# Kernel optimization log

Hardware: AMD Instinct MI355X
Metric: run time of the kernel (lower is better)

The kernel has to match this reference:

```python
import jax, jax.numpy as jnp
import numpy as np

EMBED_DIM = 768
NUM_HEADS = 12
HEAD_DIM = EMBED_DIM // NUM_HEADS


def setup_inputs() -> dict:
    key = jax.random.key(0)
    ks = jax.random.split(key, 9)
    s = 1.0 / np.sqrt(EMBED_DIM)
    inp = {
        "x": jax.random.normal(ks[0], (4, 2048, EMBED_DIM), dtype=jnp.float32),
        "W_q": jax.random.uniform(ks[1], (EMBED_DIM, EMBED_DIM), jnp.float32, -s, s),
        "b_q": jax.random.uniform(ks[2], (EMBED_DIM,), jnp.float32, -s, s),
        "W_k": jax.random.uniform(ks[3], (EMBED_DIM, EMBED_DIM), jnp.float32, -s, s),
        "b_k": jax.random.uniform(ks[4], (EMBED_DIM,), jnp.float32, -s, s),
        "W_v": jax.random.uniform(ks[5], (EMBED_DIM, EMBED_DIM), jnp.float32, -s, s),
        "b_v": jax.random.uniform(ks[6], (EMBED_DIM,), jnp.float32, -s, s),
        "W_out": jax.random.uniform(ks[7], (EMBED_DIM, EMBED_DIM), jnp.float32, -s, s),
        "b_out": jax.random.uniform(ks[8], (EMBED_DIM,), jnp.float32, -s, s),
    }
    return inp


def reference(x, W_q, b_q, W_k, b_k, W_v, b_v, W_out, b_out):
    B, N, D = x.shape
    H, Hd = NUM_HEADS, HEAD_DIM
    scale = 1.0 / jnp.sqrt(jnp.asarray(Hd, x.dtype))
    # QKV projections (torch Linear: x @ W.T + b)
    Q = (x @ W_q.T + b_q).reshape(B, N, H, Hd).transpose(0, 2, 1, 3)  # (B,H,N,Hd)
    K = (x @ W_k.T + b_k).reshape(B, N, H, Hd).transpose(0, 2, 1, 3)
    V = (x @ W_v.T + b_v).reshape(B, N, H, Hd).transpose(0, 2, 1, 3)
    scores = jnp.einsum("bhqd,bhkd->bhqk", Q, K) * scale  # (B,H,N,N)
    attn = jax.nn.softmax(scores, axis=-1)
    out = jnp.einsum("bhqk,bhkd->bhqd", attn, V)  # (B,H,N,Hd)
    out = out.transpose(0, 2, 1, 3).reshape(B, N, D)
    return out @ W_out.T + b_out
```

## Files before the change

### kernel.cpp

```cpp
#include <hip/hip_runtime.h>
#include <math.h>

#define D_EMB 768
#define SEQN 2048
#define NB 4
#define NH 12
#define HDIM 64
#define MTOT (NB*SEQN)
#define SCLQ 0.18033688011112042f

typedef unsigned int u32;
typedef unsigned short u16;
typedef short sh4 __attribute__((ext_vector_type(4)));
typedef short bf16x8 __attribute__((ext_vector_type(8)));
typedef float f32x16 __attribute__((ext_vector_type(16)));

#define MFMA32(a,b,c) __builtin_amdgcn_mfma_f32_32x32x16_bf16((a),(b),(c),0,0,0)

__device__ __forceinline__ u32 cvtpk(float a, float b){
    u32 r; asm("v_cvt_pk_bf16_f32 %0, %1, %2" : "=v"(r) : "v"(a), "v"(b)); return r;
}
__device__ __forceinline__ u32 pack_split(float v){
    u32 h = cvtpk(v, v);
    float hf = __builtin_bit_cast(float, h << 16);
    float r = v - hf;
    u32 l = cvtpk(r, r);
    return __builtin_amdgcn_perm(l, h, 0x05040100u);
}
__device__ __forceinline__ void unpack4(uint4 p, sh4& hi, sh4& lo){
    u32 h0 = __builtin_amdgcn_perm(p.y, p.x, 0x05040100u);
    u32 h1 = __builtin_amdgcn_perm(p.w, p.z, 0x05040100u);
    u32 l0 = __builtin_amdgcn_perm(p.y, p.x, 0x07060302u);
    u32 l1 = __builtin_amdgcn_perm(p.w, p.z, 0x07060302u);
    uint2 h = {h0, h1}, l = {l0, l1};
    hi = __builtin_bit_cast(sh4, h);
    lo = __builtin_bit_cast(sh4, l);
}
__device__ __forceinline__ bf16x8 ldfrag(const short* p){
    sh4 a = *(const sh4*)p;
    sh4 b = *(const sh4*)(p+4);
    return __builtin_shufflevector(a,b,0,1,2,3,4,5,6,7);
}

__global__ __launch_bounds__(256) void pack_bf(const float* __restrict__ s, u16* __restrict__ d, int n4){
    int i = blockIdx.x*256 + threadIdx.x;
    if (i >= n4) return;
    float4 v = ((const float4*)s)[i];
    uint2 o = { cvtpk(v.x, v.y), cvtpk(v.z, v.w) };
    ((uint2*)d)[i] = o;
}
__global__ __launch_bounds__(256) void pack_wbf(const float* __restrict__ w0, const float* __restrict__ w1,
                                                const float* __restrict__ w2, const float* __restrict__ w3,
                                                u16* __restrict__ d, int n4){
    const int z = blockIdx.y;
    const float* s = (z==0)?w0:(z==1)?w1:(z==2)?w2:w3;
    int i = blockIdx.x*256 + threadIdx.x;
    if (i >= n4) return;
    float4 v = ((const float4*)s)[i];
    uint2 o = { cvtpk(v.x, v.y), cvtpk(v.z, v.w) };
    ((uint2*)(d + (size_t)z*n4*4))[i] = o;
}

#define GPAD 36

__global__ __launch_bounds__(256,3) void gemm_qkv(const u16* __restrict__ X, const u16* __restrict__ Wb,
        const float* __restrict__ bq, const float* __restrict__ bk, const float* __restrict__ bv,
        u16* __restrict__ oq, u16* __restrict__ okk, u16* __restrict__ ov){
    __shared__ __align__(16) short Ahi[128][GPAD];
    __shared__ __align__(16) short Bhi[128][GPAD];

    const int tid = threadIdx.x;
    const int l = tid & 63, w = tid >> 6;
    const int lq = l & 31, g = l >> 5;
    const int wm = w >> 1, wn = w & 1;
    const int m0 = blockIdx.x * 128;
    const int n0 = blockIdx.y * 128;
    const int z  = blockIdx.z;
    const u16* W = Wb + (size_t)z * D_EMB * D_EMB;
    const float* bias = (z==0) ? bq : (z==1) ? bk : bv;
    u16* out = (z==0) ? oq : (z==1) ? okk : ov;

    f32x16 acc[2][2];
    #pragma unroll
    for (int i=0;i<2;i++)
        #pragma unroll
        for (int j=0;j<2;j++)
            #pragma unroll
            for (int r=0;r<16;r++) acc[i][j][r] = 0.f;

    const int srow = tid >> 1;
    const int skb  = (tid & 1) * 16;
    const u16* ap0 = X + (size_t)(m0+srow)*D_EMB + skb;
    const u16* wp0 = W + (size_t)(n0+srow)*D_EMB + skb;

    uint4 a0 = *(const uint4*)ap0, a1 = *(const uint4*)(ap0+8);
    uint4 w0 = *(const uint4*)wp0, w1 = *(const uint4*)(wp0+8);

    for (int k0 = 0; k0 < D_EMB; k0 += 32) {
        __syncthreads();
        {
            uint2 t;
            t.x=a0.x; t.y=a0.y; *(uint2*)&Ahi[srow][skb]    = t;
            t.x=a0.z; t.y=a0.w; *(uint2*)&Ahi[srow][skb+4]  = t;
            t.x=a1.x; t.y=a1.y; *(uint2*)&Ahi[srow][skb+8]  = t;
            t.x=a1.z; t.y=a1.w; *(uint2*)&Ahi[srow][skb+12] = t;
            t.x=w0.x; t.y=w0.y; *(uint2*)&Bhi[srow][skb]    = t;
            t.x=w0.z; t.y=w0.w; *(uint2*)&Bhi[srow][skb+4]  = t;
            t.x=w1.x; t.y=w1.y; *(uint2*)&Bhi[srow][skb+8]  = t;
            t.x=w1.z; t.y=w1.w; *(uint2*)&Bhi[srow][skb+12] = t;
        }
        if (k0 + 32 < D_EMB){
            const u16* ap = ap0 + k0 + 32;
            const u16* wp = wp0 + k0 + 32;
            a0 = *(const uint4*)ap; a1 = *(const uint4*)(ap+8);
            w0 = *(const uint4*)wp; w1 = *(const uint4*)(wp+8);
        }
        __syncthreads();
        #pragma unroll
        for (int kk=0;kk<2;kk++){
            const int kc = kk*16 + g*8;
            bf16x8 ah[2], bh[2];
            #pragma unroll
            for (int i=0;i<2;i++) ah[i] = ldfrag(&Ahi[wm*64+32*i+lq][kc]);
            #pragma unroll
            for (int j=0;j<2;j++) bh[j] = ldfrag(&Bhi[wn*64+32*j+lq][kc]);
            #pragma unroll
            for (int i=0;i<2;i++)
                #pragma unroll
                for (int j=0;j<2;j++)
                    acc[i][j] = MFMA32(ah[i], bh[j], acc[i][j]);
        }
    }

    #pragma unroll
    for (int j=0;j<2;j++){
        const int c = n0 + wn*64 + 32*j + lq;
        const float bv2 = bias[c];
        #pragma unroll
        for (int i=0;i<2;i++){
            #pragma unroll
            for (int r=0;r<16;r++){
                const int m = m0 + wm*64 + 32*i + (r&3) + 8*(r>>2) + 4*g;
                float v = acc[i][j][r] + bv2;
                if (z==0) v *= SCLQ;
                const int b = m >> 11, n = m & 2047, h = c >> 6, hd = c & 63;
                out[(((size_t)(b*NH + h))*SEQN + n)*HDIM + hd] = (u16)cvtpk(v, v);
            }
        }
    }
}

__global__ __launch_bounds__(256,3) void gemm_out(const u32* __restrict__ A, const u16* __restrict__ Wb,
        const float* __restrict__ bo, float* __restrict__ outp){
    __shared__ __align__(16) short Ahi[128][GPAD];
    __shared__ __align__(16) short Alo[128][GPAD];
    __shared__ __align__(16) short Bhi[128][GPAD];

    const int tid = threadIdx.x;
    const int l = tid & 63, w = tid >> 6;
    const int lq = l & 31, g = l >> 5;
    const int wm = w >> 1, wn = w & 1;
    const int m0 = blockIdx.x * 128;
    const int n0 = blockIdx.y * 128;
    const u16* W = Wb + (size_t)3 * D_EMB * D_EMB;

    f32x16 acc[2][2];
    #pragma unroll
    for (int i=0;i<2;i++)
        #pragma unroll
        for (int j=0;j<2;j++)
            #pragma unroll
            for (int r=0;r<16;r++) acc[i][j][r] = 0.f;

    const int srow = tid >> 1;
    const int skb  = (tid & 1) * 16;
    const u32* ap0 = A + (size_t)(m0+srow)*D_EMB + skb;
    const u16* wp0 = W + (size_t)(n0+srow)*D_EMB + skb;

    uint4 areg[4];
    uint4 w0 = *(const uint4*)wp0, w1 = *(const uint4*)(wp0+8);
    #pragma unroll
    for (int c=0;c<4;c++) areg[c] = *(const uint4*)(ap0 + 4*c);

    for (int k0 = 0; k0 < D_EMB; k0 += 32) {
        __syncthreads();
        #pragma unroll
        for (int c=0;c<4;c++){
            sh4 h, lo2; unpack4(areg[c], h, lo2);
            *(sh4*)&Ahi[srow][skb+4*c] = h;
            *(sh4*)&Alo[srow][skb+4*c] = lo2;
        }
        {
            uint2 t;
            t.x=w0.x; t.y=w0.y; *(uint2*)&Bhi[srow][skb]    = t;
            t.x=w0.z; t.y=w0.w; *(uint2*)&Bhi[srow][skb+4]  = t;
            t.x=w1.x; t.y=w1.y; *(uint2*)&Bhi[srow][skb+8]  = t;
            t.x=w1.z; t.y=w1.w; *(uint2*)&Bhi[srow][skb+12] = t;
        }
        if (k0 + 32 < D_EMB){
            const u32* ap = ap0 + k0 + 32;
            const u16* wp = wp0 + k0 + 32;
            #pragma unroll
            for (int c=0;c<4;c++) areg[c] = *(const uint4*)(ap + 4*c);
            w0 = *(const uint4*)wp; w1 = *(const uint4*)(wp+8);
        }
        __syncthreads();
        #pragma unroll
        for (int kk=0;kk<2;kk++){
            const int kc = kk*16 + g*8;
            bf16x8 ah[2], al[2], bh[2];
            #pragma unroll
            for (int i=0;i<2;i++){
                ah[i] = ldfrag(&Ahi[wm*64+32*i+lq][kc]);
                al[i] = ldfrag(&Alo[wm*64+32*i+lq][kc]);
            }
            #pragma unroll
            for (int j=0;j<2;j++) bh[j] = ldfrag(&Bhi[wn*64+32*j+lq][kc]);
            #pragma unroll
            for (int i=0;i<2;i++)
                #pragma unroll
                for (int j=0;j<2;j++){
                    acc[i][j] = MFMA32(ah[i], bh[j], acc[i][j]);
                    acc[i][j] = MFMA32(al[i], bh[j], acc[i][j]);
                }
        }
    }

    #pragma unroll
    for (int j=0;j<2;j++){
        const int c = n0 + wn*64 + 32*j + lq;
        const float bv2 = bo[c];
        #pragma unroll
        for (int i=0;i<2;i++){
            #pragma unroll
            for (int r=0;r<16;r++){
                const int m = m0 + wm*64 + 32*i + (r&3) + 8*(r>>2) + 4*g;
                outp[(size_t)m*D_EMB + c] = acc[i][j][r] + bv2;
            }
        }
    }
}

#define KB 64
#define KPAD 68
#define NT (SEQN/KB)

__global__ __launch_bounds__(256,2) void attn_bf(const u16* __restrict__ Qg,
                                                 const u16* __restrict__ Kg,
                                                 const u16* __restrict__ Vg,
                                                 u32* __restrict__ Og) {
    __shared__ __align__(16) short Khi[2][KB][KPAD];
    __shared__ __align__(16) short Vthi[2][HDIM][KPAD];

    const int tid = threadIdx.x;
    const int l = tid & 63, w = tid >> 6;
    const int lq = l & 31, g = l >> 5;
    const int qt = blockIdx.x;
    const int bh = blockIdx.y;
    const size_t base = (size_t)bh * SEQN * HDIM;
    const int qrowA = qt*256 + w*64 + lq;
    const int qrowB = qrowA + 32;

    const int key = tid >> 2, dblk = (tid & 3) * 16;
    const int hd = tid & 63, kg = tid >> 6;
    const u16* kp0 = Kg + base + (size_t)key*HDIM + dblk;
    const u16* vp0 = Vg + base + (size_t)(kg*16)*HDIM + hd;

    bf16x8 qhA[4], qhB[4];
    {
        const u16* qpA = Qg + base + (size_t)qrowA*HDIM;
        const u16* qpB = Qg + base + (size_t)qrowB*HDIM;
        #pragma unroll
        for (int kk=0;kk<4;kk++){
            qhA[kk] = __builtin_bit_cast(bf16x8, *(const uint4*)(qpA + kk*16 + g*8));
            qhB[kk] = __builtin_bit_cast(bf16x8, *(const uint4*)(qpB + kk*16 + g*8));
        }
    }

    f32x16 oA0, oA1, oB0, oB1, zro;
    #pragma unroll
    for (int r=0;r<16;r++){ oA0[r]=0.f; oA1[r]=0.f; oB0[r]=0.f; oB1[r]=0.f; zro[r]=0.f; }
    float2 lrA = {0.f, 0.f}, lrB = {0.f, 0.f};

    uint4 kra, krb;
    u32 vt[16];

    auto loadTile = [&](int t){
        const u16* kp = kp0 + (size_t)t*KB*HDIM;
        const u16* vp = vp0 + (size_t)t*KB*HDIM;
        kra = *(const uint4*)kp;
        krb = *(const uint4*)(kp+8);
        #pragma unroll
        for (int i2=0;i2<16;i2++) vt[i2] = vp[(size_t)i2*HDIM];
    };
    auto stageWrite = [&](int cb){
        uint2 t;
        t.x=kra.x; t.y=kra.y; *(uint2*)&Khi[cb][key][dblk]    = t;
        t.x=kra.z; t.y=kra.w; *(uint2*)&Khi[cb][key][dblk+4]  = t;
        t.x=krb.x; t.y=krb.y; *(uint2*)&Khi[cb][key][dblk+8]  = t;
        t.x=krb.z; t.y=krb.w; *(uint2*)&Khi[cb][key][dblk+12] = t;
        #pragma unroll
        for (int c=0;c<4;c++){
            uint2 v2;
            v2.x = __builtin_amdgcn_perm(vt[4*c+1], vt[4*c+0], 0x05040100u);
            v2.y = __builtin_amdgcn_perm(vt[4*c+3], vt[4*c+2], 0x05040100u);
            *(uint2*)&Vthi[cb][hd][kg*16+4*c] = v2;
        }
    };

    loadTile(0);
    stageWrite(0);
    loadTile(1);

    for (int kt=0; kt<NT; kt++){
        const int cb = kt & 1;
        __syncthreads();
        if (kt+1 < NT){
            stageWrite(cb^1);
            if (kt+2 < NT) loadTile(kt+2);
        }

        #pragma unroll
        for (int kb=0; kb<2; kb++){
            f32x16 sA, sB;
            __builtin_amdgcn_s_setprio(1);
            {
                bf16x8 a = ldfrag(&Khi[cb][kb*32+lq][g*8]);
                sA = MFMA32(a, qhA[0], zro);
                sB = MFMA32(a, qhB[0], zro);
            }
            #pragma unroll
            for (int kk=1;kk<4;kk++){
                bf16x8 a = ldfrag(&Khi[cb][kb*32+lq][kk*16 + g*8]);
                sA = MFMA32(a, qhA[kk], sA);
                sB = MFMA32(a, qhB[kk], sB);
            }
            __builtin_amdgcn_s_setprio(0);

            #pragma unroll
            for (int r=0;r<16;r++){ sA[r] = __builtin_amdgcn_exp2f(sA[r]); sB[r] = __builtin_amdgcn_exp2f(sB[r]); }
            #pragma unroll
            for (int r=0;r<16;r+=2){
                float2 a2 = {sA[r], sA[r+1]};
                float2 b2 = {sB[r], sB[r+1]};
                lrA += a2;
                lrB += b2;
            }

            u32 pkA[8], pkB[8];
            #pragma unroll
            for (int j=0;j<8;j++){
                pkA[j] = cvtpk(sA[2*j], sA[2*j+1]);
                pkB[j] = cvtpk(sB[2*j], sB[2*j+1]);
            }
            u32 nA0[4], nA1[4], nB0[4], nB1[4];
            #pragma unroll
            for (int a2=0;a2<2;a2++){
                #pragma unroll
                for (int c=0;c<2;c++){
                    u32 x0 = pkA[4*a2+c], y0 = pkA[4*a2+2+c];
                    asm("v_permlane32_swap_b32 %0, %1" : "+v"(x0), "+v"(y0));
                    nA0[2*a2+c] = x0; nA1[2*a2+c] = y0;
                    u32 x1 = pkB[4*a2+c], y1 = pkB[4*a2+2+c];
                    asm("v_permlane32_swap_b32 %0, %1" : "+v"(x1), "+v"(y1));
                    nB0[2*a2+c] = x1; nB1[2*a2+c] = y1;
                }
            }

            __builtin_amdgcn_s_setprio(1);
            #pragma unroll
            for (int t2=0; t2<2; t2++){
                const int kk = 2*kb + t2;
                uint4 wAv = { nA0[2*t2], nA0[2*t2+1], nA1[2*t2], nA1[2*t2+1] };
                uint4 wBv = { nB0[2*t2], nB0[2*t2+1], nB1[2*t2], nB1[2*t2+1] };
                bf16x8 pbA = __builtin_bit_cast(bf16x8, wAv);
                bf16x8 pbB = __builtin_bit_cast(bf16x8, wBv);
                const int kc = kk*16 + g*8;
                bf16x8 v0h = ldfrag(&Vthi[cb][lq][kc]);
                bf16x8 v1h = ldfrag(&Vthi[cb][32+lq][kc]);
                oA0 = MFMA32(v0h, pbA, oA0);
                oA1 = MFMA32(v1h, pbA, oA1);
                oB0 = MFMA32(v0h, pbB, oB0);
                oB1 = MFMA32(v1h, pbB, oB1);
            }
            __builtin_amdgcn_s_setprio(0);
        }
    }

    const int b = bh / NH, h = bh % NH;
    {
        float lA = lrA.x + lrA.y;
        lA += __shfl_xor(lA, 32);
        const float inv = 1.f / lA;
        u32* op = Og + ((size_t)(b*SEQN + qrowA))*D_EMB + h*HDIM;
        #pragma unroll
        for (int rq=0; rq<4; rq++){
            uint4 w0, w1;
            w0.x = pack_split(oA0[4*rq+0]*inv); w0.y = pack_split(oA0[4*rq+1]*inv);
            w0.z = pack_split(oA0[4*rq+2]*inv); w0.w = pack_split(oA0[4*rq+3]*inv);
            w1.x = pack_split(oA1[4*rq+0]*inv); w1.y = pack_split(oA1[4*rq+1]*inv);
            w1.z = pack_split(oA1[4*rq+2]*inv); w1.w = pack_split(oA1[4*rq+3]*inv);
            *(uint4*)(op + 8*rq + 4*g)      = w0;
            *(uint4*)(op + 32 + 8*rq + 4*g) = w1;
        }
    }
    {
        float lB = lrB.x + lrB.y;
        lB += __shfl_xor(lB, 32);
        const float inv = 1.f / lB;
        u32* op = Og + ((size_t)(b*SEQN + qrowB))*D_EMB + h*HDIM;
        #pragma unroll
        for (int rq=0; rq<4; rq++){
            uint4 w0, w1;
            w0.x = pack_split(oB0[4*rq+0]*inv); w0.y = pack_split(oB0[4*rq+1]*inv);
            w0.z = pack_split(oB0[4*rq+2]*inv); w0.w = pack_split(oB0[4*rq+3]*inv);
            w1.x = pack_split(oB1[4*rq+0]*inv); w1.y = pack_split(oB1[4*rq+1]*inv);
            w1.z = pack_split(oB1[4*rq+2]*inv); w1.w = pack_split(oB1[4*rq+3]*inv);
            *(uint4*)(op + 8*rq + 4*g)      = w0;
            *(uint4*)(op + 32 + 8*rq + 4*g) = w1;
        }
    }
}

extern "C" void kernel_launch(void* const* d_in, const int* in_sizes, int n_in,
                              void* d_out, int out_size, void* d_ws, size_t ws_size,
                              hipStream_t stream) {
    const float* x  = (const float*)d_in[0];
    const float* Wq = (const float*)d_in[1];
    const float* bq = (const float*)d_in[2];
    const float* Wk = (const float*)d_in[3];
    const float* bk = (const float*)d_in[4];
    const float* Wv = (const float*)d_in[5];
    const float* bv = (const float*)d_in[6];
    const float* Wo = (const float*)d_in[7];
    const float* bo = (const float*)d_in[8];

    const size_t per = (size_t)NB*NH*SEQN*HDIM;
    const size_t wplane = (size_t)D_EMB*D_EMB;
    u16* base16 = (u16*)d_ws;
    u16* Xbf = base16;
    u16* Qb  = base16 + per;
    u16* Kb  = base16 + 2*per;
    u16* Vb  = base16 + 3*per;
    u16* Wbf = base16 + 4*per;
    u32* ATpk = (u32*)(base16 + 4*per + 4*wplane);

    pack_bf<<<dim3((int)(per/4/256)), dim3(256), 0, stream>>>(x, Xbf, (int)(per/4));
    pack_wbf<<<dim3(576,4), dim3(256), 0, stream>>>(Wq, Wk, Wv, Wo, Wbf, (int)(wplane/4));

    gemm_qkv<<<dim3(MTOT/128, D_EMB/128, 3), dim3(256), 0, stream>>>(Xbf, Wbf, bq, bk, bv, Qb, Kb, Vb);

    attn_bf<<<dim3(SEQN/256, NB*NH), dim3(256), 0, stream>>>(Qb, Kb, Vb, ATpk);

    gemm_out<<<dim3(MTOT/128, D_EMB/128), dim3(256), 0, stream>>>(ATpk, Wbf, bo, (float*)d_out);
}
```

Measured before the change: 165.1 us.

## Split key tile across wave pairs in attention and reduce partial outputs via LDS

Each block now covers 128 query rows instead of 256. Pairs of waves share the same query rows, and each wave of a pair handles one 32-key half of every 64-key tile. At the end, partial O accumulators and row sums are reduced through shared memory before normalising and writing. This doubles the grid to 768 blocks and raises launch bounds to 3 blocks per SM, aiming for better occupancy and CU fill. In exchange, K/V tile loads are amortised over fewer queries, and an extra LDS reduction with syncs is added.

```diff
diff --git a/kernel.cpp b/kernel.cpp
--- a/kernel.cpp
+++ b/kernel.cpp
@@ -245,7 +245,7 @@
 #define KPAD 68
 #define NT (SEQN/KB)
 
-__global__ __launch_bounds__(256,2) void attn_bf(const u16* __restrict__ Qg,
+__global__ __launch_bounds__(256,3) void attn_bf(const u16* __restrict__ Qg,
                                                  const u16* __restrict__ Kg,
                                                  const u16* __restrict__ Vg,
                                                  u32* __restrict__ Og) {
@@ -255,10 +255,12 @@
     const int tid = threadIdx.x;
     const int l = tid & 63, w = tid >> 6;
     const int lq = l & 31, g = l >> 5;
+    const int khalf = w & 1;
+    const int pair  = w >> 1;
     const int qt = blockIdx.x;
     const int bh = blockIdx.y;
     const size_t base = (size_t)bh * SEQN * HDIM;
-    const int qrowA = qt*256 + w*64 + lq;
+    const int qrowA = qt*128 + pair*64 + lq;
     const int qrowB = qrowA + 32;
 
     const int key = tid >> 2, dblk = (tid & 3) * 16;
@@ -320,104 +322,130 @@
             if (kt+2 < NT) loadTile(kt+2);
         }
 
-        #pragma unroll
-        for (int kb=0; kb<2; kb++){
-            f32x16 sA, sB;
-            __builtin_amdgcn_s_setprio(1);
-            {
-                bf16x8 a = ldfrag(&Khi[cb][kb*32+lq][g*8]);
-                sA = MFMA32(a, qhA[0], zro);
-                sB = MFMA32(a, qhB[0], zro);
-            }
-            #pragma unroll
-            for (int kk=1;kk<4;kk++){
-                bf16x8 a = ldfrag(&Khi[cb][kb*32+lq][kk*16 + g*8]);
-                sA = MFMA32(a, qhA[kk], sA);
-                sB = MFMA32(a, qhB[kk], sB);
-            }
-            __builtin_amdgcn_s_setprio(0);
-
-            #pragma unroll
-            for (int r=0;r<16;r++){ sA[r] = __builtin_amdgcn_exp2f(sA[r]); sB[r] = __builtin_amdgcn_exp2f(sB[r]); }
-            #pragma unroll
-            for (int r=0;r<16;r+=2){
-                float2 a2 = {sA[r], sA[r+1]};
-                float2 b2 = {sB[r], sB[r+1]};
-                lrA += a2;
-                lrB += b2;
-            }
-
-            u32 pkA[8], pkB[8];
-            #pragma unroll
-            for (int j=0;j<8;j++){
-                pkA[j] = cvtpk(sA[2*j], sA[2*j+1]);
-                pkB[j] = cvtpk(sB[2*j], sB[2*j+1]);
-            }
-            u32 nA0[4], nA1[4], nB0[4], nB1[4];
-            #pragma unroll
-            for (int a2=0;a2<2;a2++){
-                #pragma unroll
-                for (int c=0;c<2;c++){
-                    u32 x0 = pkA[4*a2+c], y0 = pkA[4*a2+2+c];
-                    asm("v_permlane32_swap_b32 %0, %1" : "+v"(x0), "+v"(y0));
-                    nA0[2*a2+c] = x0; nA1[2*a2+c] = y0;
-                    u32 x1 = pkB[4*a2+c], y1 = pkB[4*a2+2+c];
-                    asm("v_permlane32_swap_b32 %0, %1" : "+v"(x1), "+v"(y1));
-                    nB0[2*a2+c] = x1; nB1[2*a2+c] = y1;
-                }
-            }
-
-            __builtin_amdgcn_s_setprio(1);
-            #pragma unroll
-            for (int t2=0; t2<2; t2++){
-                const int kk = 2*kb + t2;
-                uint4 wAv = { nA0[2*t2], nA0[2*t2+1], nA1[2*t2], nA1[2*t2+1] };
-                uint4 wBv = { nB0[2*t2], nB0[2*t2+1], nB1[2*t2], nB1[2*t2+1] };
-                bf16x8 pbA = __builtin_bit_cast(bf16x8, wAv);
-                bf16x8 pbB = __builtin_bit_cast(bf16x8, wBv);
-                const int kc = kk*16 + g*8;
-                bf16x8 v0h = ldfrag(&Vthi[cb][lq][kc]);
-                bf16x8 v1h = ldfrag(&Vthi[cb][32+lq][kc]);
-                oA0 = MFMA32(v0h, pbA, oA0);
-                oA1 = MFMA32(v1h, pbA, oA1);
-                oB0 = MFMA32(v0h, pbB, oB0);
-                oB1 = MFMA32(v1h, pbB, oB1);
-            }
-            __builtin_amdgcn_s_setprio(0);
-        }
-    }
-
-    const int b = bh / NH, h = bh % NH;
+        f32x16 sA, sB;
+        __builtin_amdgcn_s_setprio(1);
+        {
+            bf16x8 a = ldfrag(&Khi[cb][khalf*32+lq][g*8]);
+            sA = MFMA32(a, qhA[0], zro);
+            sB = MFMA32(a, qhB[0], zro);
+        }
+        #pragma unroll
+        for (int kk=1;kk<4;kk++){
+            bf16x8 a = ldfrag(&Khi[cb][khalf*32+lq][kk*16 + g*8]);
+            sA = MFMA32(a, qhA[kk], sA);
+            sB = MFMA32(a, qhB[kk], sB);
+        }
+        __builtin_amdgcn_s_setprio(0);
+
+        #pragma unroll
+        for (int r=0;r<16;r++){ sA[r] = __builtin_amdgcn_exp2f(sA[r]); sB[r] = __builtin_amdgcn_exp2f(sB[r]); }
+        #pragma unroll
+        for (int r=0;r<16;r+=2){
+            float2 a2 = {sA[r], sA[r+1]};
+            float2 b2 = {sB[r], sB[r+1]};
+            lrA += a2;
+            lrB += b2;
+        }
+
+        u32 pkA[8], pkB[8];
+        #pragma unroll
+        for (int j=0;j<8;j++){
+            pkA[j] = cvtpk(sA[2*j], sA[2*j+1]);
+            pkB[j] = cvtpk(sB[2*j], sB[2*j+1]);
+        }
+        u32 nA0[4], nA1[4], nB0[4], nB1[4];
+        #pragma unroll
+        for (int a2=0;a2<2;a2++){
+            #pragma unroll
+            for (int c=0;c<2;c++){
+                u32 x0 = pkA[4*a2+c], y0 = pkA[4*a2+2+c];
+                asm("v_permlane32_swap_b32 %0, %1" : "+v"(x0), "+v"(y0));
+                nA0[2*a2+c] = x0; nA1[2*a2+c] = y0;
+                u32 x1 = pkB[4*a2+c], y1 = pkB[4*a2+2+c];
+                asm("v_permlane32_swap_b32 %0, %1" : "+v"(x1), "+v"(y1));
+                nB0[2*a2+c] = x1; nB1[2*a2+c] = y1;
+            }
+        }
+
+        __builtin_amdgcn_s_setprio(1);
+        #pragma unroll
+        for (int t2=0; t2<2; t2++){
+            const int kk = 2*khalf + t2;
+            uint4 wAv = { nA0[2*t2], nA0[2*t2+1], nA1[2*t2], nA1[2*t2+1] };
+            uint4 wBv = { nB0[2*t2], nB0[2*t2+1], nB1[2*t2], nB1[2*t2+1] };
+            bf16x8 pbA = __builtin_bit_cast(bf16x8, wAv);
+            bf16x8 pbB = __builtin_bit_cast(bf16x8, wBv);
+            const int kc = kk*16 + g*8;
+            bf16x8 v0h = ldfrag(&Vthi[cb][lq][kc]);
+            bf16x8 v1h = ldfrag(&Vthi[cb][32+lq][kc]);
+            oA0 = MFMA32(v0h, pbA, oA0);
+            oA1 = MFMA32(v1h, pbA, oA1);
+            oB0 = MFMA32(v0h, pbB, oB0);
+            oB1 = MFMA32(v1h, pbB, oB1);
+        }
+        __builtin_amdgcn_s_setprio(0);
+    }
+
+    __syncthreads();
     {
-        float lA = lrA.x + lrA.y;
+        float* reg = pair ? (float*)&Vthi[0][0][0] : (float*)&Khi[0][0][0];
+        float* slot = reg + (size_t)l*68;
+        if (khalf){
+            #pragma unroll
+            for (int r=0;r<16;r++){
+                slot[r]    = oA0[r];
+                slot[16+r] = oA1[r];
+                slot[32+r] = oB0[r];
+                slot[48+r] = oB1[r];
+            }
+            slot[64] = lrA.x + lrA.y;
+            slot[65] = lrB.x + lrB.y;
+        }
+    }
+    __syncthreads();
+    if (!khalf){
+        const float* reg = pair ? (const float*)&Vthi[0][0][0] : (const float*)&Khi[0][0][0];
+        const float* slot = reg + (size_t)l*68;
+        #pragma unroll
+        for (int r=0;r<16;r++){
+            oA0[r] += slot[r];
+            oA1[r] += slot[16+r];
+            oB0[r] += slot[32+r];
+            oB1[r] += slot[48+r];
+        }
+        float lA = lrA.x + lrA.y + slot[64];
+        float lB = lrB.x + lrB.y + slot[65];
         lA += __shfl_xor(lA, 32);
-        const float inv = 1.f / lA;
-        u32* op = Og + ((size_t)(b*SEQN + qrowA))*D_EMB + h*HDIM;
-        #pragma unroll
-        for (int rq=0; rq<4; rq++){
-            uint4 w0, w1;
-            w0.x = pack_split(oA0[4*rq+0]*inv); w0.y = pack_split(oA0[4*rq+1]*inv);
-            w0.z = pack_split(oA0[4*rq+2]*inv); w0.w = pack_split(oA0[4*rq+3]*inv);
-            w1.x = pack_split(oA1[4*rq+0]*inv); w1.y = pack_split(oA1[4*rq+1]*inv);
-            w1.z = pack_split(oA1[4*rq+2]*inv); w1.w = pack_split(oA1[4*rq+3]*inv);
-            *(uint4*)(op + 8*rq + 4*g)      = w0;
-            *(uint4*)(op + 32 + 8*rq + 4*g) = w1;
-        }
-    }
-    {
-        float lB = lrB.x + lrB.y;
         lB += __shfl_xor(lB, 32);
-        const float inv = 1.f / lB;
-        u32* op = Og + ((size_t)(b*SEQN + qrowB))*D_EMB + h*HDIM;
-        #pragma unroll
-        for (int rq=0; rq<4; rq++){
-            uint4 w0, w1;
-            w0.x = pack_split(oB0[4*rq+0]*inv); w0.y = pack_split(oB0[4*rq+1]*inv);
-            w0.z = pack_split(oB0[4*rq+2]*inv); w0.w = pack_split(oB0[4*rq+3]*inv);
-            w1.x = pack_split(oB1[4*rq+0]*inv); w1.y = pack_split(oB1[4*rq+1]*inv);
-            w1.z = pack_split(oB1[4*rq+2]*inv); w1.w = pack_split(oB1[4*rq+3]*inv);
-            *(uint4*)(op + 8*rq + 4*g)      = w0;
-            *(uint4*)(op + 32 + 8*rq + 4*g) = w1;
+
+        const int b = bh / NH, h = bh % NH;
+        {
+            const float inv = 1.f / lA;
+            u32* op = Og + ((size_t)(b*SEQN + qrowA))*D_EMB + h*HDIM;
+            #pragma unroll
+            for (int rq=0; rq<4; rq++){
+                uint4 w0, w1;
+                w0.x = pack_split(oA0[4*rq+0]*inv); w0.y = pack_split(oA0[4*rq+1]*inv);
+                w0.z = pack_split(oA0[4*rq+2]*inv); w0.w = pack_split(oA0[4*rq+3]*inv);
+                w1.x = pack_split(oA1[4*rq+0]*inv); w1.y = pack_split(oA1[4*rq+1]*inv);
+                w1.z = pack_split(oA1[4*rq+2]*inv); w1.w = pack_split(oA1[4*rq+3]*inv);
+                *(uint4*)(op + 8*rq + 4*g)      = w0;
+                *(uint4*)(op + 32 + 8*rq + 4*g) = w1;
+            }
+        }
+        {
+            const float inv = 1.f / lB;
+            u32* op = Og + ((size_t)(b*SEQN + qrowB))*D_EMB + h*HDIM;
+            #pragma unroll
+            for (int rq=0; rq<4; rq++){
+                uint4 w0, w1;
+                w0.x = pack_split(oB0[4*rq+0]*inv); w0.y = pack_split(oB0[4*rq+1]*inv);
+                w0.z = pack_split(oB0[4*rq+2]*inv); w0.w = pack_split(oB0[4*rq+3]*inv);
+                w1.x = pack_split(oB1[4*rq+0]*inv); w1.y = pack_split(oB1[4*rq+1]*inv);
+                w1.z = pack_split(oB1[4*rq+2]*inv); w1.w = pack_split(oB1[4*rq+3]*inv);
+                *(uint4*)(op + 8*rq + 4*g)      = w0;
+                *(uint4*)(op + 32 + 8*rq + 4*g) = w1;
+            }
         }
     }
 }
@@ -450,7 +478,7 @@
 
     gemm_qkv<<<dim3(MTOT/128, D_EMB/128, 3), dim3(256), 0, stream>>>(Xbf, Wbf, bq, bk, bv, Qb, Kb, Vb);
 
-    attn_bf<<<dim3(SEQN/256, NB*NH), dim3(256), 0, stream>>>(Qb, Kb, Vb, ATpk);
+    attn_bf<<<dim3(SEQN/128, NB*NH), dim3(256), 0, stream>>>(Qb, Kb, Vb, ATpk);
 
     gemm_out<<<dim3(MTOT/128, D_EMB/128), dim3(256), 0, stream>>>(ATpk, Wbf, bo, (float*)d_out);
 }
```

New measurement: 168.5 us. +2.0%, slower.
